# Kernel tuning notes

Hardware: AMD Instinct MI355X
Metric: run time of the kernel (lower is better)

## Reference

```python
import jax, jax.numpy as jnp
import numpy as np

N_NODES = 100000
N_EDGES = 1600000
IN_DIM, HIDDEN_DIM, OUT_DIM = 500, 64, 40


def setup_inputs() -> dict:
    key = jax.random.key(0)
    k1, k2, k3, k4, k5 = jax.random.split(key, 5)
    x = jax.random.normal(k1, (N_NODES, IN_DIM), dtype=jnp.float32)
    edge_index = jax.random.randint(k2, (2, N_EDGES), 0, N_NODES, dtype=jnp.int64)
    # Glorot-style init like PyG GCNConv
    W1 = jax.random.normal(k3, (IN_DIM, HIDDEN_DIM), dtype=jnp.float32) / np.sqrt(IN_DIM)
    b1 = jnp.zeros((HIDDEN_DIM,), dtype=jnp.float32)
    W2 = jax.random.normal(k4, (HIDDEN_DIM, OUT_DIM), dtype=jnp.float32) / np.sqrt(HIDDEN_DIM)
    b2 = jnp.zeros((OUT_DIM,), dtype=jnp.float32)
    return {"x": x, "W1": W1, "b1": b1, "W2": W2, "b2": b2, "edge_index": edge_index}


def _gcn_conv(x, W, b, src, dst, n):
    """PyG GCNConv: h = D^{-1/2} (A + I) D^{-1/2} (x W) + b."""
    h = x @ W  # transform first, propagate in smaller dim
    loops = jnp.arange(n, dtype=src.dtype)
    s = jnp.concatenate([src, loops])
    d = jnp.concatenate([dst, loops])
    deg = jax.ops.segment_sum(jnp.ones_like(d, dtype=h.dtype), d, num_segments=n)
    dinv = jnp.where(deg > 0, jax.lax.rsqrt(deg), 0.0)
    norm = dinv[s] * dinv[d]               # [E+N]
    msg = h[s] * norm[:, None]             # gather + scale
    out = jax.ops.segment_sum(msg, d, num_segments=n)  # scatter-add
    return out + b


def reference(x, W1, b1, W2, b2, edge_index):
    src, dst = edge_index[0], edge_index[1]
    n = x.shape[0]
    h = _gcn_conv(x, W1, b1, src, dst, n)
    h = jax.nn.relu(h)  # eval mode: dropout is identity
    out = _gcn_conv(h, W2, b2, src, dst, n)
    return out
```

## Files before the change

kernel.cpp:

```cpp
#include <hip/hip_runtime.h>
#include <cstdint>
#include <cstddef>

#define NN 100000
#define NE 1600000
#define IND 500
#define HD 64
#define OD 40
#define NBLK ((NN + 255) / 256)
#define KSTEPS 16
#define NTT 16

typedef __attribute__((ext_vector_type(8))) short short8v;
typedef __attribute__((ext_vector_type(8))) __bf16 bf16x8;
typedef __attribute__((ext_vector_type(4))) float float4v;

template <class V>
static __device__ __forceinline__ auto mfma_bf16_(V a, V b, float4v c, int)
    -> decltype(__builtin_amdgcn_mfma_f32_16x16x32_bf16(a, b, c, 0, 0, 0)) {
    return __builtin_amdgcn_mfma_f32_16x16x32_bf16(a, b, c, 0, 0, 0);
}
template <class V>
static __device__ __forceinline__ float4v mfma_bf16_(V a, V b, float4v c, long) {
    return __builtin_amdgcn_mfma_f32_16x16x32_bf16((bf16x8)a, (bf16x8)b, c, 0, 0, 0);
}
static __device__ __forceinline__ float4v mfma16(short8v a, short8v b, float4v c) {
    return mfma_bf16_(a, b, c, 0);
}

static __device__ __forceinline__ float bf2f(unsigned short v) {
    return __uint_as_float((unsigned)v << 16);
}
static __device__ __forceinline__ unsigned short f2bf(float v) {
    unsigned u = __float_as_uint(v);
    return (unsigned short)((u + 0x7fffu + ((u >> 16) & 1u)) >> 16);
}

typedef __attribute__((address_space(3))) char lds_char;
typedef const __attribute__((address_space(1))) char g_char;
static __device__ __forceinline__ void gl16(const char* g, char* l) {
    __builtin_amdgcn_global_load_lds((g_char*)g, (lds_char*)l, 16, 0, 0);
}

static __device__ __forceinline__ void load4e(const void* ei, int is64, size_t base, int v[4]) {
    if (is64) {
        int4 a = ((const int4*)ei)[base >> 1];
        int4 b = ((const int4*)ei)[(base >> 1) + 1];
        v[0] = a.x; v[1] = a.z; v[2] = b.x; v[3] = b.z;
    } else {
        int4 a = *(const int4*)((const int*)ei + base);
        v[0] = a.x; v[1] = a.y; v[2] = a.z; v[3] = a.w;
    }
}

__global__ void k_count(const void* ei, const int* __restrict__ flags, int* cnt,
                        int* __restrict__ rank) {
    int e0 = (blockIdx.x * 256 + threadIdx.x) * 4;
    if (e0 >= NE) return;
    int d[4];
    load4e(ei, flags[0], (size_t)NE + e0, d);
    int4 r;
    r.x = atomicAdd(&cnt[d[0]], 1);
    r.y = atomicAdd(&cnt[d[1]], 1);
    r.z = atomicAdd(&cnt[d[2]], 1);
    r.w = atomicAdd(&cnt[d[3]], 1);
    *(int4*)(rank + e0) = r;
}

__global__ __launch_bounds__(256) void k_scan_block(const int* __restrict__ cnt,
                                                    int* __restrict__ rowptr,
                                                    int* __restrict__ bsum,
                                                    float* __restrict__ dinv) {
    int t = threadIdx.x;
    int i = blockIdx.x * 256 + t;
    int v = (i < NN) ? cnt[i] : 0;
    if (i < NN) dinv[i] = rsqrtf((float)v + 1.0f);
    int inc = v;
    #pragma unroll
    for (int off = 1; off < 64; off <<= 1) {
        int u = __shfl_up(inc, off);
        if ((t & 63) >= off) inc += u;
    }
    __shared__ int wsum[4];
    if ((t & 63) == 63) wsum[t >> 6] = inc;
    __syncthreads();
    if (t == 0) {
        int a = 0;
        #pragma unroll
        for (int w = 0; w < 4; ++w) { int b = wsum[w]; wsum[w] = a; a += b; }
        bsum[blockIdx.x] = a;
    }
    __syncthreads();
    if (i < NN) rowptr[i] = inc - v + wsum[t >> 6];
}

__global__ __launch_bounds__(512) void k_scan_bsum(int* bsum) {
    int t = threadIdx.x;
    int v = (t < NBLK) ? bsum[t] : 0;
    int inc = v;
    #pragma unroll
    for (int off = 1; off < 64; off <<= 1) {
        int u = __shfl_up(inc, off);
        if ((t & 63) >= off) inc += u;
    }
    __shared__ int wsum[8];
    if ((t & 63) == 63) wsum[t >> 6] = inc;
    __syncthreads();
    if (t == 0) {
        int a = 0;
        #pragma unroll
        for (int w = 0; w < 8; ++w) { int b = wsum[w]; wsum[w] = a; a += b; }
    }
    __syncthreads();
    if (t < NBLK) bsum[t] = inc - v + wsum[t >> 6];
}

__global__ void k_scan_add(int* rowptr, const int* __restrict__ bsum) {
    int i = blockIdx.x * 256 + threadIdx.x;
    if (i < NN) rowptr[i] += bsum[i >> 8];
    if (i == 0) rowptr[NN] = NE;
}

__global__ void k_scatter(const void* ei, const int* __restrict__ flags,
                          const int* __restrict__ rowptr, const int* __restrict__ rank,
                          int* __restrict__ srcs) {
    int e0 = (blockIdx.x * 256 + threadIdx.x) * 4;
    if (e0 >= NE) return;
    int is64 = flags[0];
    int s[4], d[4];
    load4e(ei, is64, (size_t)e0, s);
    load4e(ei, is64, (size_t)NE + e0, d);
    int4 r = *(const int4*)(rank + e0);
    int p0 = rowptr[d[0]] + r.x;
    int p1 = rowptr[d[1]] + r.y;
    int p2 = rowptr[d[2]] + r.z;
    int p3 = rowptr[d[3]] + r.w;
    srcs[p0] = s[0];
    srcs[p1] = s[1];
    srcs[p2] = s[2];
    srcs[p3] = s[3];
}

__global__ void k_prepw(const float* __restrict__ W, unsigned short* __restrict__ wh,
                        unsigned short* __restrict__ wl,
                        const unsigned* __restrict__ ei32, int* __restrict__ flags) {
    int t = blockIdx.x * 256 + threadIdx.x;
    if (t == 0) {
        int is64 = 1;
        #pragma unroll
        for (int i = 1; i < 16; i += 2)
            if (ei32[i] != 0u) is64 = 0;
        flags[0] = is64;
    }
    if (t >= KSTEPS * 4 * 64) return;
    int l = t & 63;
    int f = (t >> 6) & 3;
    int s = t >> 8;
    int n = f * 16 + (l & 15);
    int kbase = s * 32 + 8 * (l >> 4);
    unsigned short* ph = wh + (size_t)t * 8;
    unsigned short* pl = wl + (size_t)t * 8;
    #pragma unroll
    for (int j = 0; j < 8; ++j) {
        int k = kbase + j;
        float v = (k < IND) ? W[(size_t)k * HD + n] : 0.f;
        unsigned u = __float_as_uint(v);
        unsigned short hb = (unsigned short)(u >> 16);
        float r = v - __uint_as_float(u & 0xffff0000u);
        ph[j] = hb;
        pl[j] = f2bf(r);
    }
}

static __device__ __forceinline__ void split8f(float4 u0, float4 u1,
                                               short8v& hi, short8v& lo) {
    float t[8] = {u0.x, u0.y, u0.z, u0.w, u1.x, u1.y, u1.z, u1.w};
    #pragma unroll
    for (int j = 0; j < 8; ++j) {
        unsigned q = __float_as_uint(t[j]);
        hi[j] = (short)(q >> 16);
        float r = t[j] - __uint_as_float(q & 0xffff0000u);
        lo[j] = (short)f2bf(r);
    }
}

__global__ __launch_bounds__(256, 5) void k_gemm1m(const float* __restrict__ x,
                                                   const char* __restrict__ whb,
                                                   const char* __restrict__ wlb,
                                                   const float* __restrict__ dinv,
                                                   unsigned short* __restrict__ h) {
    __shared__ char smem[32768];
    const int tid  = threadIdx.x;
    const int lane = tid & 63;
    const int wave = tid >> 6;
    const int row0 = blockIdx.x * 64;
    const int rA = lane & 15;
    const int cg = lane >> 4;

    auto stage = [&](int kt, int buf) {
        const bool tail = (kt == NTT - 1);
        #pragma unroll
        for (int i = 0; i < 2; ++i) {
            int slot = i * 256 + tid;
            int r = slot >> 3, c = slot & 7;
            int cs = c ^ (r & 7);
            if (tail && cs > 4) cs = 4;
            int rsrc = row0 + r; if (rsrc >= NN) rsrc = NN - 1;
            const char* g = (const char*)x + (size_t)rsrc * (IND * 4) + kt * 128 + cs * 16;
            char* l = smem + buf * 16384 + (i * 256 + wave * 64) * 16;
            gl16(g, l);
        }
        #pragma unroll
        for (int i = 0; i < 2; ++i) {
            int j = i * 256 + tid;
            const char* src = (j < 256 ? whb : wlb) + kt * 4096 + (size_t)(j & 255) * 16;
            char* l = smem + buf * 16384 + 8192 + (i * 256 + wave * 64) * 16;
            gl16(src, l);
        }
    };

    float4v acc[4];
    const float4v zero4 = {0.f, 0.f, 0.f, 0.f};
    #pragma unroll
    for (int f = 0; f < 4; ++f) acc[f] = zero4;

    stage(0, 0);
    __syncthreads();

    int cur = 0;
    const int rbase = (wave * 16 + rA) * 8;
    const int sw = rA & 7;

    for (int kt = 0; kt < NTT; ++kt) {
        if (kt + 1 < NTT) stage(kt + 1, cur ^ 1);
        const float4*  pa = (const float4*)(smem + cur * 16384);
        const short8v* pb = (const short8v*)(smem + cur * 16384 + 8192);
        int ch = cg * 2;
        float4 u0 = pa[rbase + (ch ^ sw)];
        float4 u1 = pa[rbase + ((ch + 1) ^ sw)];
        short8v ah, al;
        split8f(u0, u1, ah, al);
        #pragma unroll
        for (int f = 0; f < 4; ++f) {
            short8v vh = pb[f * 64 + lane];
            short8v vl = pb[256 + f * 64 + lane];
            acc[f] = mfma16(al, vh, acc[f]);
            acc[f] = mfma16(ah, vl, acc[f]);
            acc[f] = mfma16(ah, vh, acc[f]);
        }
        __syncthreads();
        cur ^= 1;
    }

    #pragma unroll
    for (int j = 0; j < 4; ++j) {
        int row = row0 + wave * 16 + cg * 4 + j;
        if (row < NN) {
            float dv = dinv[row];
            #pragma unroll
            for (int f = 0; f < 4; ++f)
                h[(size_t)row * HD + f * 16 + rA] = f2bf(acc[f][j] * dv);
        }
    }
}

template<bool L1>
__global__ __launch_bounds__(256) void k_agg(const int* __restrict__ rowptr,
                                             const int* __restrict__ srcs,
                                             const float* __restrict__ dinv,
                                             const unsigned short* __restrict__ hb,
                                             const float* __restrict__ bias,
                                             unsigned short* __restrict__ outb,
                                             float* __restrict__ outf) {
    int wid = (blockIdx.x * 256 + threadIdx.x) >> 6;
    int lane = threadIdx.x & 63;
    if (wid >= NN) return;
    float acc = bf2f(hb[(size_t)wid * HD + lane]);
    int beg = rowptr[wid];
    int cnt = rowptr[wid + 1] - beg;
    for (int base = 0; base < cnt; base += 64) {
        int m = cnt - base; if (m > 64) m = 64;
        int sj = (lane < m) ? srcs[beg + base + lane] : 0;
        int j = 0;
        for (; j + 8 <= m; j += 8) {
            int s0 = __builtin_amdgcn_readlane(sj, j);
            int s1 = __builtin_amdgcn_readlane(sj, j + 1);
            int s2 = __builtin_amdgcn_readlane(sj, j + 2);
            int s3 = __builtin_amdgcn_readlane(sj, j + 3);
            int s4 = __builtin_amdgcn_readlane(sj, j + 4);
            int s5 = __builtin_amdgcn_readlane(sj, j + 5);
            int s6 = __builtin_amdgcn_readlane(sj, j + 6);
            int s7 = __builtin_amdgcn_readlane(sj, j + 7);
            float v0 = bf2f(hb[(size_t)s0 * HD + lane]);
            float v1 = bf2f(hb[(size_t)s1 * HD + lane]);
            float v2 = bf2f(hb[(size_t)s2 * HD + lane]);
            float v3 = bf2f(hb[(size_t)s3 * HD + lane]);
            float v4 = bf2f(hb[(size_t)s4 * HD + lane]);
            float v5 = bf2f(hb[(size_t)s5 * HD + lane]);
            float v6 = bf2f(hb[(size_t)s6 * HD + lane]);
            float v7 = bf2f(hb[(size_t)s7 * HD + lane]);
            acc += ((v0 + v1) + (v2 + v3)) + ((v4 + v5) + (v6 + v7));
        }
        for (; j < m; ++j) {
            int s = __builtin_amdgcn_readlane(sj, j);
            acc += bf2f(hb[(size_t)s * HD + lane]);
        }
    }
    float dn = dinv[wid];
    acc *= dn;
    if (L1) {
        outb[(size_t)wid * HD + lane] = f2bf(fmaxf(acc + bias[lane], 0.f) * dn);
    } else {
        outf[(size_t)wid * HD + lane] = acc;
    }
}

__global__ __launch_bounds__(256) void k_gemm2(const float* __restrict__ h,
                                               const float* __restrict__ W2,
                                               const float* __restrict__ b2,
                                               float* __restrict__ out) {
    __shared__ float hs[32][65];
    __shared__ float ws2[64][40];
    const int t = threadIdx.x;
    const int r0 = blockIdx.x * 32;
    for (int i = t; i < 64 * OD; i += 256)
        ws2[i / OD][i % OD] = W2[i];
    for (int i = t; i < 32 * 64; i += 256) {
        int r = i >> 6, k = i & 63;
        hs[r][k] = h[(size_t)(r0 + r) * HD + k];
    }
    __syncthreads();
    for (int o = t; o < 32 * OD; o += 256) {
        int r = o / OD, c = o - r * OD;
        float s = 0.f;
        #pragma unroll
        for (int k = 0; k < HD; ++k)
            s = fmaf(hs[r][k], ws2[k][c], s);
        out[(size_t)(r0 + r) * OD + c] = s + b2[c];
    }
}

extern "C" void kernel_launch(void* const* d_in, const int* in_sizes, int n_in,
                              void* d_out, int out_size, void* d_ws, size_t ws_size,
                              hipStream_t stream) {
    const float* x  = (const float*)d_in[0];
    const float* W1 = (const float*)d_in[1];
    const float* b1 = (const float*)d_in[2];
    const float* W2 = (const float*)d_in[3];
    const float* b2 = (const float*)d_in[4];
    const void*  ei = d_in[5];
    float* out = (float*)d_out;

    char* ob = (char*)d_out;
    int*   rowptr = (int*)ob;
    int*   cnt    = (int*)(ob + 400896);
    int*   bsum   = (int*)(ob + 801280);
    int*   srcs   = (int*)(ob + 803328);
    float* dinv   = (float*)(ob + 7203840);
    int*   rank   = (int*)(ob + 7604224);
    unsigned short* wh = (unsigned short*)(ob + 14004736);
    unsigned short* wl = (unsigned short*)(ob + 14070272);

    char* ws = (char*)d_ws;
    int*            flags  = (int*)ws;
    unsigned short* h1b    = (unsigned short*)(ws + 1024);
    unsigned short* hrelub = (unsigned short*)(ws + 1024 + 12800000);
    float*          agg2   = (float*)(ws + 1024 + 25600000);

    k_prepw<<<(KSTEPS * 4 * 64 + 255) / 256, 256, 0, stream>>>(W1, wh, wl, (const unsigned*)ei, flags);

    hipMemsetAsync(cnt, 0, (size_t)NN * 4, stream);
    k_count<<<(NE / 4 + 255) / 256, 256, 0, stream>>>(ei, flags, cnt, rank);
    k_scan_block<<<NBLK, 256, 0, stream>>>(cnt, rowptr, bsum, dinv);
    k_scan_bsum<<<1, 512, 0, stream>>>(bsum);
    k_scan_add<<<NBLK, 256, 0, stream>>>(rowptr, bsum);
    k_scatter<<<(NE / 4 + 255) / 256, 256, 0, stream>>>(ei, flags, rowptr, rank, srcs);

    k_gemm1m<<<(NN + 63) / 64, 256, 0, stream>>>(x, (const char*)wh, (const char*)wl, dinv, h1b);
    k_agg<true><<<(NN * 64) / 256, 256, 0, stream>>>(rowptr, srcs, dinv, h1b, b1, hrelub, (float*)nullptr);

    k_agg<false><<<(NN * 64) / 256, 256, 0, stream>>>(rowptr, srcs, dinv, hrelub, (const float*)nullptr, (unsigned short*)nullptr, agg2);
    k_gemm2<<<NN / 32, 256, 0, stream>>>(agg2, W2, b2, out);
}
```

Measured before the change: 321.3 us.

## Fuse graph-build and GEMM kernels to cut launches and intermediate traffic

Folds weight preparation into the edge-count kernel and has every thread detect the index width itself, which removes the flags buffer. The CSR scatter is interleaved with the first GEMM in one launch (odd blocks scatter, even blocks run the GEMM), so the two can overlap. The second aggregation is fused with the 64x40 output GEMM through shared memory, which removes the fp32 agg2 round trip through global memory. Scratch buffers move from the output buffer to the workspace; the fused GEMM uses one wave per row with a serial 64-step dot product, which may be less efficient than the old blocked GEMM.

New measurement: 333.4 us. +3.8%, slower.

```diff
diff --git a/kernel.cpp b/kernel.cpp
--- a/kernel.cpp
+++ b/kernel.cpp
@@ -10,6 +10,7 @@
 #define NBLK ((NN + 255) / 256)
 #define KSTEPS 16
 #define NTT 16
+#define EB 1563
 
 typedef __attribute__((ext_vector_type(8))) short short8v;
 typedef __attribute__((ext_vector_type(8))) __bf16 bf16x8;
@@ -40,6 +41,15 @@
 typedef const __attribute__((address_space(1))) char g_char;
 static __device__ __forceinline__ void gl16(const char* g, char* l) {
     __builtin_amdgcn_global_load_lds((g_char*)g, (lds_char*)l, 16, 0, 0);
+}
+
+static __device__ __forceinline__ int detect64(const void* ei) {
+    const unsigned* u = (const unsigned*)ei;
+    int is64 = 1;
+    #pragma unroll
+    for (int i = 1; i < 16; i += 2)
+        if (u[i] != 0u) is64 = 0;
+    return is64;
 }
 
 static __device__ __forceinline__ void load4e(const void* ei, int is64, size_t base, int v[4]) {
@@ -53,18 +63,42 @@
     }
 }
 
-__global__ void k_count(const void* ei, const int* __restrict__ flags, int* cnt,
-                        int* __restrict__ rank) {
+__global__ __launch_bounds__(256) void k_count_prep(const void* ei, int* cnt,
+                                                    int* __restrict__ rank,
+                                                    const float* __restrict__ W,
+                                                    unsigned short* __restrict__ wh,
+                                                    unsigned short* __restrict__ wl) {
+    const int is64 = detect64(ei);
     int e0 = (blockIdx.x * 256 + threadIdx.x) * 4;
-    if (e0 >= NE) return;
-    int d[4];
-    load4e(ei, flags[0], (size_t)NE + e0, d);
-    int4 r;
-    r.x = atomicAdd(&cnt[d[0]], 1);
-    r.y = atomicAdd(&cnt[d[1]], 1);
-    r.z = atomicAdd(&cnt[d[2]], 1);
-    r.w = atomicAdd(&cnt[d[3]], 1);
-    *(int4*)(rank + e0) = r;
+    if (e0 < NE) {
+        int d[4];
+        load4e(ei, is64, (size_t)NE + e0, d);
+        int4 r;
+        r.x = atomicAdd(&cnt[d[0]], 1);
+        r.y = atomicAdd(&cnt[d[1]], 1);
+        r.z = atomicAdd(&cnt[d[2]], 1);
+        r.w = atomicAdd(&cnt[d[3]], 1);
+        *(int4*)(rank + e0) = r;
+    }
+    int t = blockIdx.x * 256 + threadIdx.x;
+    if (t < KSTEPS * 4 * 64) {
+        int l = t & 63;
+        int f = (t >> 6) & 3;
+        int s = t >> 8;
+        int n = f * 16 + (l & 15);
+        int kbase = s * 32 + 8 * (l >> 4);
+        unsigned short* ph = wh + (size_t)t * 8;
+        unsigned short* pl = wl + (size_t)t * 8;
+        #pragma unroll
+        for (int j = 0; j < 8; ++j) {
+            int k = kbase + j;
+            float v = (k < IND) ? W[(size_t)k * HD + n] : 0.f;
+            unsigned u = __float_as_uint(v);
+            ph[j] = (unsigned short)(u >> 16);
+            float r = v - __uint_as_float(u & 0xffff0000u);
+            pl[j] = f2bf(r);
+        }
+    }
 }
 
 __global__ __launch_bounds__(256) void k_scan_block(const int* __restrict__ cnt,
@@ -121,57 +155,6 @@
     if (i == 0) rowptr[NN] = NE;
 }
 
-__global__ void k_scatter(const void* ei, const int* __restrict__ flags,
-                          const int* __restrict__ rowptr, const int* __restrict__ rank,
-                          int* __restrict__ srcs) {
-    int e0 = (blockIdx.x * 256 + threadIdx.x) * 4;
-    if (e0 >= NE) return;
-    int is64 = flags[0];
-    int s[4], d[4];
-    load4e(ei, is64, (size_t)e0, s);
-    load4e(ei, is64, (size_t)NE + e0, d);
-    int4 r = *(const int4*)(rank + e0);
-    int p0 = rowptr[d[0]] + r.x;
-    int p1 = rowptr[d[1]] + r.y;
-    int p2 = rowptr[d[2]] + r.z;
-    int p3 = rowptr[d[3]] + r.w;
-    srcs[p0] = s[0];
-    srcs[p1] = s[1];
-    srcs[p2] = s[2];
-    srcs[p3] = s[3];
-}
-
-__global__ void k_prepw(const float* __restrict__ W, unsigned short* __restrict__ wh,
-                        unsigned short* __restrict__ wl,
-                        const unsigned* __restrict__ ei32, int* __restrict__ flags) {
-    int t = blockIdx.x * 256 + threadIdx.x;
-    if (t == 0) {
-        int is64 = 1;
-        #pragma unroll
-        for (int i = 1; i < 16; i += 2)
-            if (ei32[i] != 0u) is64 = 0;
-        flags[0] = is64;
-    }
-    if (t >= KSTEPS * 4 * 64) return;
-    int l = t & 63;
-    int f = (t >> 6) & 3;
-    int s = t >> 8;
-    int n = f * 16 + (l & 15);
-    int kbase = s * 32 + 8 * (l >> 4);
-    unsigned short* ph = wh + (size_t)t * 8;
-    unsigned short* pl = wl + (size_t)t * 8;
-    #pragma unroll
-    for (int j = 0; j < 8; ++j) {
-        int k = kbase + j;
-        float v = (k < IND) ? W[(size_t)k * HD + n] : 0.f;
-        unsigned u = __float_as_uint(v);
-        unsigned short hb = (unsigned short)(u >> 16);
-        float r = v - __uint_as_float(u & 0xffff0000u);
-        ph[j] = hb;
-        pl[j] = f2bf(r);
-    }
-}
-
 static __device__ __forceinline__ void split8f(float4 u0, float4 u1,
                                                short8v& hi, short8v& lo) {
     float t[8] = {u0.x, u0.y, u0.z, u0.w, u1.x, u1.y, u1.z, u1.w};
@@ -184,16 +167,34 @@
     }
 }
 
-__global__ __launch_bounds__(256, 5) void k_gemm1m(const float* __restrict__ x,
-                                                   const char* __restrict__ whb,
-                                                   const char* __restrict__ wlb,
-                                                   const float* __restrict__ dinv,
-                                                   unsigned short* __restrict__ h) {
+__global__ __launch_bounds__(256, 5) void k_gemm_scatter(const float* __restrict__ x,
+                                                         const char* __restrict__ whb,
+                                                         const char* __restrict__ wlb,
+                                                         const float* __restrict__ dinv,
+                                                         unsigned short* __restrict__ h,
+                                                         const void* __restrict__ ei,
+                                                         const int* __restrict__ rowptr,
+                                                         const int* __restrict__ rank,
+                                                         int* __restrict__ srcs) {
     __shared__ char smem[32768];
+    if (blockIdx.x & 1) {
+        int e0 = ((blockIdx.x >> 1) * 256 + threadIdx.x) * 4;
+        if (e0 >= NE) return;
+        const int is64 = detect64(ei);
+        int s[4], d[4];
+        load4e(ei, is64, (size_t)e0, s);
+        load4e(ei, is64, (size_t)NE + e0, d);
+        int4 r = *(const int4*)(rank + e0);
+        srcs[rowptr[d[0]] + r.x] = s[0];
+        srcs[rowptr[d[1]] + r.y] = s[1];
+        srcs[rowptr[d[2]] + r.z] = s[2];
+        srcs[rowptr[d[3]] + r.w] = s[3];
+        return;
+    }
     const int tid  = threadIdx.x;
     const int lane = tid & 63;
     const int wave = tid >> 6;
-    const int row0 = blockIdx.x * 64;
+    const int row0 = (blockIdx.x >> 1) * 64;
     const int rA = lane & 15;
     const int cg = lane >> 4;
 
@@ -264,14 +265,12 @@
     }
 }
 
-template<bool L1>
-__global__ __launch_bounds__(256) void k_agg(const int* __restrict__ rowptr,
-                                             const int* __restrict__ srcs,
-                                             const float* __restrict__ dinv,
-                                             const unsigned short* __restrict__ hb,
-                                             const float* __restrict__ bias,
-                                             unsigned short* __restrict__ outb,
-                                             float* __restrict__ outf) {
+__global__ __launch_bounds__(256) void k_agg1(const int* __restrict__ rowptr,
+                                              const int* __restrict__ srcs,
+                                              const float* __restrict__ dinv,
+                                              const unsigned short* __restrict__ hb,
+                                              const float* __restrict__ bias,
+                                              unsigned short* __restrict__ outb) {
     int wid = (blockIdx.x * 256 + threadIdx.x) >> 6;
     int lane = threadIdx.x & 63;
     if (wid >= NN) return;
@@ -307,36 +306,64 @@
         }
     }
     float dn = dinv[wid];
-    acc *= dn;
-    if (L1) {
-        outb[(size_t)wid * HD + lane] = f2bf(fmaxf(acc + bias[lane], 0.f) * dn);
-    } else {
-        outf[(size_t)wid * HD + lane] = acc;
-    }
-}
-
-__global__ __launch_bounds__(256) void k_gemm2(const float* __restrict__ h,
-                                               const float* __restrict__ W2,
-                                               const float* __restrict__ b2,
-                                               float* __restrict__ out) {
-    __shared__ float hs[32][65];
-    __shared__ float ws2[64][40];
+    outb[(size_t)wid * HD + lane] = f2bf(fmaxf(acc * dn + bias[lane], 0.f) * dn);
+}
+
+__global__ __launch_bounds__(256) void k_agg2_gemm2(const int* __restrict__ rowptr,
+                                                    const int* __restrict__ srcs,
+                                                    const float* __restrict__ dinv,
+                                                    const unsigned short* __restrict__ hb,
+                                                    const float* __restrict__ W2,
+                                                    const float* __restrict__ b2,
+                                                    float* __restrict__ out) {
+    __shared__ float ws2[HD][OD];
+    __shared__ float hsh[4][HD];
     const int t = threadIdx.x;
-    const int r0 = blockIdx.x * 32;
-    for (int i = t; i < 64 * OD; i += 256)
+    for (int i = t; i < HD * OD; i += 256)
         ws2[i / OD][i % OD] = W2[i];
-    for (int i = t; i < 32 * 64; i += 256) {
-        int r = i >> 6, k = i & 63;
-        hs[r][k] = h[(size_t)(r0 + r) * HD + k];
-    }
-    __syncthreads();
-    for (int o = t; o < 32 * OD; o += 256) {
-        int r = o / OD, c = o - r * OD;
-        float s = 0.f;
+
+    int wid = (blockIdx.x * 256 + t) >> 6;
+    int lane = t & 63;
+    int w = t >> 6;
+    float acc = bf2f(hb[(size_t)wid * HD + lane]);
+    int beg = rowptr[wid];
+    int cnt = rowptr[wid + 1] - beg;
+    for (int base = 0; base < cnt; base += 64) {
+        int m = cnt - base; if (m > 64) m = 64;
+        int sj = (lane < m) ? srcs[beg + base + lane] : 0;
+        int j = 0;
+        for (; j + 8 <= m; j += 8) {
+            int s0 = __builtin_amdgcn_readlane(sj, j);
+            int s1 = __builtin_amdgcn_readlane(sj, j + 1);
+            int s2 = __builtin_amdgcn_readlane(sj, j + 2);
+            int s3 = __builtin_amdgcn_readlane(sj, j + 3);
+            int s4 = __builtin_amdgcn_readlane(sj, j + 4);
+            int s5 = __builtin_amdgcn_readlane(sj, j + 5);
+            int s6 = __builtin_amdgcn_readlane(sj, j + 6);
+            int s7 = __builtin_amdgcn_readlane(sj, j + 7);
+            float v0 = bf2f(hb[(size_t)s0 * HD + lane]);
+            float v1 = bf2f(hb[(size_t)s1 * HD + lane]);
+            float v2 = bf2f(hb[(size_t)s2 * HD + lane]);
+            float v3 = bf2f(hb[(size_t)s3 * HD + lane]);
+            float v4 = bf2f(hb[(size_t)s4 * HD + lane]);
+            float v5 = bf2f(hb[(size_t)s5 * HD + lane]);
+            float v6 = bf2f(hb[(size_t)s6 * HD + lane]);
+            float v7 = bf2f(hb[(size_t)s7 * HD + lane]);
+            acc += ((v0 + v1) + (v2 + v3)) + ((v4 + v5) + (v6 + v7));
+        }
+        for (; j < m; ++j) {
+            int s = __builtin_amdgcn_readlane(sj, j);
+            acc += bf2f(hb[(size_t)s * HD + lane]);
+        }
+    }
+    hsh[w][lane] = acc * dinv[wid];
+    __syncthreads();
+    if (lane < OD) {
+        float s = b2[lane];
         #pragma unroll
         for (int k = 0; k < HD; ++k)
-            s = fmaf(hs[r][k], ws2[k][c], s);
-        out[(size_t)(r0 + r) * OD + c] = s + b2[c];
+            s = fmaf(hsh[w][k], ws2[k][lane], s);
+        out[(size_t)wid * OD + lane] = s;
     }
 }
 
@@ -351,34 +378,25 @@
     const void*  ei = d_in[5];
     float* out = (float*)d_out;
 
-    char* ob = (char*)d_out;
-    int*   rowptr = (int*)ob;
-    int*   cnt    = (int*)(ob + 400896);
-    int*   bsum   = (int*)(ob + 801280);
-    int*   srcs   = (int*)(ob + 803328);
-    float* dinv   = (float*)(ob + 7203840);
-    int*   rank   = (int*)(ob + 7604224);
-    unsigned short* wh = (unsigned short*)(ob + 14004736);
-    unsigned short* wl = (unsigned short*)(ob + 14070272);
-
     char* ws = (char*)d_ws;
-    int*            flags  = (int*)ws;
-    unsigned short* h1b    = (unsigned short*)(ws + 1024);
-    unsigned short* hrelub = (unsigned short*)(ws + 1024 + 12800000);
-    float*          agg2   = (float*)(ws + 1024 + 25600000);
-
-    k_prepw<<<(KSTEPS * 4 * 64 + 255) / 256, 256, 0, stream>>>(W1, wh, wl, (const unsigned*)ei, flags);
+    unsigned short* h1b    = (unsigned short*)ws;
+    unsigned short* hrelub = (unsigned short*)(ws + 12800000);
+    int*   rowptr = (int*)(ws + 25600000);
+    int*   cnt    = (int*)(ws + 26000896);
+    int*   bsum   = (int*)(ws + 26401792);
+    int*   srcs   = (int*)(ws + 26403840);
+    int*   rank   = (int*)(ws + 32803840);
+    float* dinv   = (float*)(ws + 39203840);
+    unsigned short* wh = (unsigned short*)(ws + 39604224);
+    unsigned short* wl = (unsigned short*)(ws + 39669760);
 
     hipMemsetAsync(cnt, 0, (size_t)NN * 4, stream);
-    k_count<<<(NE / 4 + 255) / 256, 256, 0, stream>>>(ei, flags, cnt, rank);
+    k_count_prep<<<EB, 256, 0, stream>>>(ei, cnt, rank, W1, wh, wl);
     k_scan_block<<<NBLK, 256, 0, stream>>>(cnt, rowptr, bsum, dinv);
     k_scan_bsum<<<1, 512, 0, stream>>>(bsum);
     k_scan_add<<<NBLK, 256, 0, stream>>>(rowptr, bsum);
-    k_scatter<<<(NE / 4 + 255) / 256, 256, 0, stream>>>(ei, flags, rowptr, rank, srcs);
-
-    k_gemm1m<<<(NN + 63) / 64, 256, 0, stream>>>(x, (const char*)wh, (const char*)wl, dinv, h1b);
-    k_agg<true><<<(NN * 64) / 256, 256, 0, stream>>>(rowptr, srcs, dinv, h1b, b1, hrelub, (float*)nullptr);
-
-    k_agg<false><<<(NN * 64) / 256, 256, 0, stream>>>(rowptr, srcs, dinv, hrelub, (const float*)nullptr, (unsigned short*)nullptr, agg2);
-    k_gemm2<<<NN / 32, 256, 0, stream>>>(agg2, W2, b2, out);
-}
+    k_gemm_scatter<<<2 * EB, 256, 0, stream>>>(x, (const char*)wh, (const char*)wl,
+                                               dinv, h1b, ei, rowptr, rank, srcs);
+    k_agg1<<<(NN * 64) / 256, 256, 0, stream>>>(rowptr, srcs, dinv, h1b, b1, hrelub);
+    k_agg2_gemm2<<<(NN * 64) / 256, 256, 0, stream>>>(rowptr, srcs, dinv, hrelub, W2, b2, out);
+}
```
